# Optimization experiments

Measured on AMD Instinct MI355X. Metric: run time of the kernel, lower is better.

Reference implementation:

```python
import jax, jax.numpy as jnp
import numpy as np

NUM_HEADS = 8
HEAD_DIM = 16  # hidden_size 128 / 8 heads
SCALE = float(np.sqrt(HEAD_DIM))


def setup_inputs() -> dict:
    key = jax.random.key(0)
    k1, k2, k3, k4 = jax.random.split(key, 4)
    B, N, H = 1, 50000, 128
    E = 800000
    q = jax.random.normal(k1, (B, N, H), dtype=jnp.float32)
    k = jax.random.normal(k2, (B, N, H), dtype=jnp.float32)
    v = jax.random.normal(k3, (B, N, H), dtype=jnp.float32)
    edge_index = jax.random.randint(k4, (2, E), 0, N, dtype=jnp.int64)
    return {"q": q, "k": k, "v": v, "edge_index": edge_index}


def reference(q, k, v, edge_index):
    B, N, H = q.shape
    total = B * N
    qh = q.reshape(total, NUM_HEADS, HEAD_DIM)
    kh = k.reshape(total, NUM_HEADS, HEAD_DIM)
    vh = v.reshape(total, NUM_HEADS, HEAD_DIM)
    src_idx = edge_index[0]
    dst_idx = edge_index[1]
    src = kh[src_idx]          # [E, heads, d]
    dest = qh[dst_idx]         # [E, heads, d]
    # per-edge scaled dot score, clamped then exponentiated
    score = jnp.sum(src * dest / SCALE, axis=-1, keepdims=True)  # [E, heads, 1]
    score = jnp.exp(jnp.clip(score, -5.0, 5.0))
    msg = vh[src_idx] * score  # [E, heads, d]
    wV = jax.ops.segment_sum(msg, dst_idx, num_segments=total)    # [total, heads, d]
    Z = jax.ops.segment_sum(score, dst_idx, num_segments=total)   # [total, heads, 1]
    x = wV / (Z + 1e-6)
    return x.reshape(B, N, NUM_HEADS * HEAD_DIM)
```

## Files before the change

kernel.cpp:

```cpp
#include <hip/hip_runtime.h>

#define HID 128
#define CHUNK 16384
#define CSHIFT 14
#define MAXW 25088

typedef unsigned short u16;
typedef unsigned int u32;

__device__ __forceinline__ float lof(u32 w) { return __uint_as_float(w << 16); }
__device__ __forceinline__ float hif(u32 w) { return __uint_as_float(w & 0xFFFF0000u); }
__device__ __forceinline__ u16 f2bf(float f) {
    u32 x = __float_as_uint(f);
    return (u16)((x + 0x7FFF + ((x >> 16) & 1)) >> 16);
}

__global__ __launch_bounds__(1024) void hist_kernel(const int* __restrict__ ei,
        u32* __restrict__ Hp, u16* __restrict__ lrank, int E, int W) {
    __shared__ u32 hcnt[MAXW];
    int c = blockIdx.x;
    for (int j = threadIdx.x; j < W; j += 1024) hcnt[j] = 0;
    __syncthreads();
    int beg = c << CSHIFT;
    int end = min(E, beg + CHUNK);
    for (int i = beg + (int)threadIdx.x; i < end; i += 1024) {
        int d = ei[E + i];
        u32 sh = (u32)(d & 1) << 4;
        u32 old = atomicAdd(&hcnt[d >> 1], 1u << sh);
        lrank[i] = (u16)((old >> sh) & 0xFFFFu);
    }
    __syncthreads();
    for (int j = threadIdx.x; j < W; j += 1024) Hp[(size_t)c * W + j] = hcnt[j];
}

__global__ __launch_bounds__(1024) void scan_fused_kernel(u32* __restrict__ Hp,
        int* __restrict__ offsets, int* __restrict__ partials, int W, int NB, int N) {
    __shared__ int sdata[1024];
    int tid = threadIdx.x;
    int j = blockIdx.x * 1024 + tid;
    u32 lo = 0, hi = 0;
    if (j < W) {
        int c = 0;
        for (; c + 8 <= NB; c += 8) {
            u32 w[8];
#pragma unroll
            for (int t = 0; t < 8; t++) w[t] = Hp[(size_t)(c + t) * W + j];
#pragma unroll
            for (int t = 0; t < 8; t++) {
                Hp[(size_t)(c + t) * W + j] = lo | (hi << 16);
                lo += w[t] & 0xFFFFu;
                hi += w[t] >> 16;
            }
        }
        for (; c < NB; c++) {
            size_t idx = (size_t)c * W + j;
            u32 w = Hp[idx];
            Hp[idx] = lo | (hi << 16);
            lo += w & 0xFFFFu;
            hi += w >> 16;
        }
    }
    int s = (int)(lo + hi);
    sdata[tid] = s;
    __syncthreads();
    for (int off = 1; off < 1024; off <<= 1) {
        int x = sdata[tid];
        int y = (tid >= off) ? sdata[tid - off] : 0;
        __syncthreads();
        sdata[tid] = x + y;
        __syncthreads();
    }
    int excl = sdata[tid] - s;
    if (j < W) {
        int n0 = 2 * j, n1 = 2 * j + 1;
        offsets[n0] = excl;
        if (n1 < N) offsets[n1] = excl + (int)lo;
    }
    if (tid == 1023) partials[blockIdx.x] = sdata[1023];
}

__global__ void scanC_kernel(int* __restrict__ offsets, const int* __restrict__ partials,
                             int M, int E, int nbA) {
    __shared__ int sp[256];
    int tid = threadIdx.x;
    if (tid == 0) {
        int run = 0;
        for (int i = 0; i < nbA; i++) { sp[i] = run; run += partials[i]; }
    }
    __syncthreads();
    int idx = blockIdx.x * blockDim.x + tid;
    if (idx < M) offsets[idx] += sp[idx >> 11];
    if (idx == 0) offsets[M] = E;
}

__global__ void packscatter_kernel(const float* __restrict__ k, const float* __restrict__ v,
                                   u16* __restrict__ kv, const int* __restrict__ ei,
                                   const u32* __restrict__ Hp, const u16* __restrict__ lrank,
                                   const int* __restrict__ offsets, u16* __restrict__ srcs,
                                   int N, int E, int W, int packBlocks) {
    if ((int)blockIdx.x < packBlocks) {
        int g = blockIdx.x * 256 + threadIdx.x;
        int node = g >> 6, l = g & 63;
        if (node >= N) return;
        float2 kk = ((const float2*)(k + (long long)node * HID))[l];
        float2 vv = ((const float2*)(v + (long long)node * HID))[l];
        ushort4 o;
        o.x = f2bf(kk.x * 0.25f);
        o.y = f2bf(kk.y * 0.25f);
        o.z = f2bf(vv.x);
        o.w = f2bf(vv.y);
        ((ushort4*)(kv + (long long)node * 256))[l] = o;
    } else {
        int e = (blockIdx.x - packBlocks) * 256 + threadIdx.x;
        if (e >= E) return;
        int c = e >> CSHIFT;
        int d = ei[E + e];
        u32 sh = (u32)(d & 1) << 4;
        u32 b = (Hp[(size_t)c * W + (d >> 1)] >> sh) & 0xFFFFu;
        int pos = offsets[d] + (int)b + (int)lrank[e];
        srcs[pos] = (u16)ei[e];
    }
}

__global__ __launch_bounds__(128) void reduce_packed(
        const float* __restrict__ q, const u16* __restrict__ kv,
        const int* __restrict__ offsets, const u16* __restrict__ srcs,
        float* __restrict__ out, int N) {
    int node = blockIdx.x * 2 + (threadIdx.x >> 6);
    if (node >= N) return;
    int l = threadIdx.x & 63;
    int m = l & 31;
    int half = l >> 5;

    float4 qv = ((const float4*)(q + (long long)node * HID))[m];
    const char* kvb = (const char*)kv;
    u32 laneoff = (u32)m << 4;
    float4 acc = make_float4(0.0f, 0.0f, 0.0f, 0.0f);
    float z = 0.0f;

    int beg = offsets[node];
    int end = offsets[node + 1];
    int i = beg;

#define GLOAD(s_) (*(const uint4*)(kvb + (((u32)(s_) << 9) + laneoff)))

    for (; i + 8 <= end; i += 8) {
        u32 sA0 = srcs[i + 0], sB0 = srcs[i + 1];
        u32 sA1 = srcs[i + 2], sB1 = srcs[i + 3];
        u32 sA2 = srcs[i + 4], sB2 = srcs[i + 5];
        u32 sA3 = srcs[i + 6], sB3 = srcs[i + 7];
        uint4 a0 = GLOAD(half ? sB0 : sA0);
        uint4 a1 = GLOAD(half ? sB1 : sA1);
        uint4 a2 = GLOAD(half ? sB2 : sA2);
        uint4 a3 = GLOAD(half ? sB3 : sA3);

        float p0 = lof(a0.x) * qv.x + hif(a0.x) * qv.y + lof(a0.z) * qv.z + hif(a0.z) * qv.w;
        float p1 = lof(a1.x) * qv.x + hif(a1.x) * qv.y + lof(a1.z) * qv.z + hif(a1.z) * qv.w;
        float p2 = lof(a2.x) * qv.x + hif(a2.x) * qv.y + lof(a2.z) * qv.z + hif(a2.z) * qv.w;
        float p3 = lof(a3.x) * qv.x + hif(a3.x) * qv.y + lof(a3.z) * qv.z + hif(a3.z) * qv.w;

        p0 += __shfl_xor(p0, 1); p1 += __shfl_xor(p1, 1);
        p2 += __shfl_xor(p2, 1); p3 += __shfl_xor(p3, 1);
        p0 += __shfl_xor(p0, 2); p1 += __shfl_xor(p1, 2);
        p2 += __shfl_xor(p2, 2); p3 += __shfl_xor(p3, 2);

        float c0 = __expf(fminf(fmaxf(p0, -5.0f), 5.0f));
        float c1 = __expf(fminf(fmaxf(p1, -5.0f), 5.0f));
        float c2 = __expf(fminf(fmaxf(p2, -5.0f), 5.0f));
        float c3 = __expf(fminf(fmaxf(p3, -5.0f), 5.0f));

        acc.x += lof(a0.y) * c0 + lof(a1.y) * c1 + lof(a2.y) * c2 + lof(a3.y) * c3;
        acc.y += hif(a0.y) * c0 + hif(a1.y) * c1 + hif(a2.y) * c2 + hif(a3.y) * c3;
        acc.z += lof(a0.w) * c0 + lof(a1.w) * c1 + lof(a2.w) * c2 + lof(a3.w) * c3;
        acc.w += hif(a0.w) * c0 + hif(a1.w) * c1 + hif(a2.w) * c2 + hif(a3.w) * c3;
        z += c0 + c1 + c2 + c3;
    }
    for (; i < end; i += 2) {
        int idx = i + half;
        bool ok = idx < end;
        u32 s = srcs[ok ? idx : i];
        uint4 a = GLOAD(s);
        float p = lof(a.x) * qv.x + hif(a.x) * qv.y + lof(a.z) * qv.z + hif(a.z) * qv.w;
        p += __shfl_xor(p, 1);
        p += __shfl_xor(p, 2);
        float c = __expf(fminf(fmaxf(p, -5.0f), 5.0f));
        c = ok ? c : 0.0f;
        acc.x += lof(a.y) * c;
        acc.y += hif(a.y) * c;
        acc.z += lof(a.w) * c;
        acc.w += hif(a.w) * c;
        z += c;
    }
#undef GLOAD

    acc.x += __shfl_xor(acc.x, 32);
    acc.y += __shfl_xor(acc.y, 32);
    acc.z += __shfl_xor(acc.z, 32);
    acc.w += __shfl_xor(acc.w, 32);
    z     += __shfl_xor(z, 32);

    if (half == 0) {
        float inv = 1.0f / (z + 1e-6f);
        ((float4*)(out + (long long)node * HID))[m] =
            make_float4(acc.x * inv, acc.y * inv, acc.z * inv, acc.w * inv);
    }
}


__global__ void count_kernel(const int* __restrict__ ei, int* __restrict__ counts,
                             int* __restrict__ pos, int E) {
    int e = blockIdx.x * blockDim.x + threadIdx.x;
    if (e < E) pos[e] = atomicAdd(&counts[ei[E + e]], 1);
}

__global__ void fill_kernel(const int* __restrict__ ei, const int* __restrict__ offsets,
                            const int* __restrict__ pos, int* __restrict__ srcs, int E) {
    int e = blockIdx.x * blockDim.x + threadIdx.x;
    if (e < E) srcs[offsets[ei[E + e]] + pos[e]] = ei[e];
}

__global__ __launch_bounds__(256) void reduce_f32(
        const float* __restrict__ q, const float* __restrict__ k,
        const float* __restrict__ v, const int* __restrict__ offsets,
        const int* __restrict__ srcs, float* __restrict__ out, int N) {
    int node = blockIdx.x * 4 + (threadIdx.x >> 6);
    if (node >= N) return;
    int l = threadIdx.x & 63;
    float2 qv = ((const float2*)(q + (long long)node * HID))[l];
    float accx = 0.0f, accy = 0.0f, z = 0.0f;
    int beg = offsets[node], end = offsets[node + 1];
    for (int i = beg; i < end; i++) {
        int s = srcs[i];
        float2 kk = ((const float2*)(k + (long long)s * HID))[l];
        float2 vv = ((const float2*)(v + (long long)s * HID))[l];
        float p = (kk.x * qv.x + kk.y * qv.y) * 0.25f;
        p += __shfl_xor(p, 1);
        p += __shfl_xor(p, 2);
        p += __shfl_xor(p, 4);
        float c = __expf(fminf(fmaxf(p, -5.0f), 5.0f));
        accx += vv.x * c; accy += vv.y * c; z += c;
    }
    float inv = 1.0f / (z + 1e-6f);
    ((float2*)(out + (long long)node * HID))[l] = make_float2(accx * inv, accy * inv);
}

__global__ void scanA_kernel(const u32* __restrict__ counts, int* __restrict__ offsets,
                             int* __restrict__ partials, int M) {
    __shared__ int sdata[256];
    int tid = threadIdx.x;
    int base = blockIdx.x * 2048 + tid * 8;
    int v[8];
    int tsum = 0;
    for (int j = 0; j < 8; j++) {
        int idx = base + j;
        v[j] = (idx < M) ? (int)counts[idx] : 0;
        tsum += v[j];
    }
    sdata[tid] = tsum;
    __syncthreads();
    for (int off = 1; off < 256; off <<= 1) {
        int x = sdata[tid];
        int y = (tid >= off) ? sdata[tid - off] : 0;
        __syncthreads();
        sdata[tid] = x + y;
        __syncthreads();
    }
    int excl = sdata[tid] - tsum;
    for (int j = 0; j < 8; j++) {
        int idx = base + j;
        if (idx < M) offsets[idx] = excl;
        excl += v[j];
    }
    if (tid == 255) partials[blockIdx.x] = sdata[255];
}

extern "C" void kernel_launch(void* const* d_in, const int* in_sizes, int n_in,
                              void* d_out, int out_size, void* d_ws, size_t ws_size,
                              hipStream_t stream) {
    const float* q = (const float*)d_in[0];
    const float* k = (const float*)d_in[1];
    const float* v = (const float*)d_in[2];
    const int* ei = (const int*)d_in[3];
    float* out = (float*)d_out;

    int E = in_sizes[3] / 2;
    int N = in_sizes[0] / HID;

    int eblocks = (E + 255) / 256;
    int nbA = (N + 2047) / 2048;
    int nblocksN = (N + 255) / 256;

    int W = (N + 1) / 2;
    int NB = (E + CHUNK - 1) >> CSHIFT;
    int nbF = (W + 1023) / 1024;

    size_t kv_bytes = (size_t)N * 256 * sizeof(u16);
    size_t need = kv_bytes + ((size_t)NB * W + N + 1 + 256) * 4
                + 2 * ((size_t)E + 8) * 2 + 64;

    bool primary = (W <= MAXW) && (nbF <= 256) && (ws_size >= need);

    if (primary) {
        u16* kv = (u16*)d_ws;
        u32* Hp = (u32*)((char*)d_ws + kv_bytes);
        int* offsets = (int*)(Hp + (size_t)NB * W);
        int* partials = offsets + N + 1;
        u16* lrank = (u16*)(partials + 256);
        u16* srcs = lrank + ((E + 8) & ~1);

        int packBlocks = (N * 64 + 255) / 256;

        hist_kernel<<<NB, 1024, 0, stream>>>(ei, Hp, lrank, E, W);
        scan_fused_kernel<<<nbF, 1024, 0, stream>>>(Hp, offsets, partials, W, NB, N);
        scanC_kernel<<<nblocksN, 256, 0, stream>>>(offsets, partials, N, E, nbF);
        packscatter_kernel<<<packBlocks + eblocks, 256, 0, stream>>>(
            k, v, kv, ei, Hp, lrank, offsets, srcs, N, E, W, packBlocks);
        int rgrid = (N + 1) / 2;
        reduce_packed<<<rgrid, 128, 0, stream>>>(q, kv, offsets, srcs, out, N);
    } else {
        int* counts = (int*)d_ws;
        int* offsets = counts + N;
        int* partials = offsets + N + 1;
        int* pos = partials + 256;
        int* srcs = pos + E;

        hipMemsetAsync(counts, 0, (size_t)N * sizeof(int), stream);
        count_kernel<<<eblocks, 256, 0, stream>>>(ei, counts, pos, E);
        scanA_kernel<<<nbA, 256, 0, stream>>>((const u32*)counts, offsets, partials, N);
        scanC_kernel<<<nblocksN, 256, 0, stream>>>(offsets, partials, N, E, nbA);
        fill_kernel<<<eblocks, 256, 0, stream>>>(ei, offsets, pos, srcs, E);
        int rgrid = (N + 3) / 4;
        reduce_f32<<<rgrid, 256, 0, stream>>>(q, k, v, offsets, srcs, out, N);
    }
}
```

Before: 111.2 us.

## Split histogram per chunk into two halves and fuse k/v packing into it

The per-chunk histogram kernel now runs two blocks per edge chunk, each owning half of the packed destination counter range, so each block uses half the LDS (about 50KB instead of 100KB). That lets more blocks fit per CU and raises histogram parallelism. The bf16 packing of k/v moves from the scatter kernel into the histogram launch, so packing overlaps with histogramming and the scatter kernel is left doing only the scatter. The cost is that each edge's destination is read twice and filtered by range in the histogram blocks.

Result: faster. 104.8 us (-5.7%).

```diff
diff --git a/kernel.cpp b/kernel.cpp
--- a/kernel.cpp
+++ b/kernel.cpp
@@ -4,6 +4,7 @@
 #define CHUNK 16384
 #define CSHIFT 14
 #define MAXW 25088
+#define WH 12544
 
 typedef unsigned short u16;
 typedef unsigned int u32;
@@ -15,22 +16,46 @@
     return (u16)((x + 0x7FFF + ((x >> 16) & 1)) >> 16);
 }
 
-__global__ __launch_bounds__(1024) void hist_kernel(const int* __restrict__ ei,
-        u32* __restrict__ Hp, u16* __restrict__ lrank, int E, int W) {
-    __shared__ u32 hcnt[MAXW];
-    int c = blockIdx.x;
-    for (int j = threadIdx.x; j < W; j += 1024) hcnt[j] = 0;
-    __syncthreads();
-    int beg = c << CSHIFT;
-    int end = min(E, beg + CHUNK);
-    for (int i = beg + (int)threadIdx.x; i < end; i += 1024) {
-        int d = ei[E + i];
-        u32 sh = (u32)(d & 1) << 4;
-        u32 old = atomicAdd(&hcnt[d >> 1], 1u << sh);
-        lrank[i] = (u16)((old >> sh) & 0xFFFFu);
-    }
-    __syncthreads();
-    for (int j = threadIdx.x; j < W; j += 1024) Hp[(size_t)c * W + j] = hcnt[j];
+__global__ __launch_bounds__(1024) void histpack_kernel(
+        const int* __restrict__ ei, u32* __restrict__ Hp, u16* __restrict__ lrank,
+        const float* __restrict__ kin, const float* __restrict__ vin, u16* __restrict__ kv,
+        int E, int W, int N, int histBlocks) {
+    __shared__ u32 hcnt[WH];
+    if ((int)blockIdx.x < histBlocks) {
+        int c = blockIdx.x >> 1;
+        int h = blockIdx.x & 1;
+        int Wh = (W + 1) >> 1;
+        int base = h * Wh;
+        int wlen = min(Wh, W - base);
+        for (int j = threadIdx.x; j < wlen; j += 1024) hcnt[j] = 0;
+        __syncthreads();
+        int beg = c << CSHIFT;
+        int end = min(E, beg + CHUNK);
+        for (int i = beg + (int)threadIdx.x; i < end; i += 1024) {
+            int d = ei[E + i];
+            int w = d >> 1;
+            if (w >= base && w < base + wlen) {
+                u32 sh = (u32)(d & 1) << 4;
+                u32 old = atomicAdd(&hcnt[w - base], 1u << sh);
+                lrank[i] = (u16)((old >> sh) & 0xFFFFu);
+            }
+        }
+        __syncthreads();
+        for (int j = threadIdx.x; j < wlen; j += 1024)
+            Hp[(size_t)c * W + base + j] = hcnt[j];
+    } else {
+        int g = ((int)blockIdx.x - histBlocks) * 1024 + (int)threadIdx.x;
+        int node = g >> 6, l = g & 63;
+        if (node >= N) return;
+        float2 kk = ((const float2*)(kin + (long long)node * HID))[l];
+        float2 vv = ((const float2*)(vin + (long long)node * HID))[l];
+        ushort4 o;
+        o.x = f2bf(kk.x * 0.25f);
+        o.y = f2bf(kk.y * 0.25f);
+        o.z = f2bf(vv.x);
+        o.w = f2bf(vv.y);
+        ((ushort4*)(kv + (long long)node * 256))[l] = o;
+    }
 }
 
 __global__ __launch_bounds__(1024) void scan_fused_kernel(u32* __restrict__ Hp,
@@ -93,33 +118,17 @@
     if (idx == 0) offsets[M] = E;
 }
 
-__global__ void packscatter_kernel(const float* __restrict__ k, const float* __restrict__ v,
-                                   u16* __restrict__ kv, const int* __restrict__ ei,
-                                   const u32* __restrict__ Hp, const u16* __restrict__ lrank,
-                                   const int* __restrict__ offsets, u16* __restrict__ srcs,
-                                   int N, int E, int W, int packBlocks) {
-    if ((int)blockIdx.x < packBlocks) {
-        int g = blockIdx.x * 256 + threadIdx.x;
-        int node = g >> 6, l = g & 63;
-        if (node >= N) return;
-        float2 kk = ((const float2*)(k + (long long)node * HID))[l];
-        float2 vv = ((const float2*)(v + (long long)node * HID))[l];
-        ushort4 o;
-        o.x = f2bf(kk.x * 0.25f);
-        o.y = f2bf(kk.y * 0.25f);
-        o.z = f2bf(vv.x);
-        o.w = f2bf(vv.y);
-        ((ushort4*)(kv + (long long)node * 256))[l] = o;
-    } else {
-        int e = (blockIdx.x - packBlocks) * 256 + threadIdx.x;
-        if (e >= E) return;
-        int c = e >> CSHIFT;
-        int d = ei[E + e];
-        u32 sh = (u32)(d & 1) << 4;
-        u32 b = (Hp[(size_t)c * W + (d >> 1)] >> sh) & 0xFFFFu;
-        int pos = offsets[d] + (int)b + (int)lrank[e];
-        srcs[pos] = (u16)ei[e];
-    }
+__global__ void scatter_kernel(const int* __restrict__ ei, const u32* __restrict__ Hp,
+                               const u16* __restrict__ lrank, const int* __restrict__ offsets,
+                               u16* __restrict__ srcs, int E, int W) {
+    int e = blockIdx.x * blockDim.x + threadIdx.x;
+    if (e >= E) return;
+    int c = e >> CSHIFT;
+    int d = ei[E + e];
+    u32 sh = (u32)(d & 1) << 4;
+    u32 b = (Hp[(size_t)c * W + (d >> 1)] >> sh) & 0xFFFFu;
+    int pos = offsets[d] + (int)b + (int)lrank[e];
+    srcs[pos] = (u16)ei[e];
 }
 
 __global__ __launch_bounds__(128) void reduce_packed(
@@ -298,7 +307,7 @@
     size_t need = kv_bytes + ((size_t)NB * W + N + 1 + 256) * 4
                 + 2 * ((size_t)E + 8) * 2 + 64;
 
-    bool primary = (W <= MAXW) && (nbF <= 256) && (ws_size >= need);
+    bool primary = (((W + 1) >> 1) <= WH) && (nbF <= 256) && (ws_size >= need);
 
     if (primary) {
         u16* kv = (u16*)d_ws;
@@ -308,13 +317,14 @@
         u16* lrank = (u16*)(partials + 256);
         u16* srcs = lrank + ((E + 8) & ~1);
 
-        int packBlocks = (N * 64 + 255) / 256;
-
-        hist_kernel<<<NB, 1024, 0, stream>>>(ei, Hp, lrank, E, W);
+        int histBlocks = NB * 2;
+        int packBlocks = (N * 64 + 1023) / 1024;
+
+        histpack_kernel<<<histBlocks + packBlocks, 1024, 0, stream>>>(
+            ei, Hp, lrank, k, v, kv, E, W, N, histBlocks);
         scan_fused_kernel<<<nbF, 1024, 0, stream>>>(Hp, offsets, partials, W, NB, N);
         scanC_kernel<<<nblocksN, 256, 0, stream>>>(offsets, partials, N, E, nbF);
-        packscatter_kernel<<<packBlocks + eblocks, 256, 0, stream>>>(
-            k, v, kv, ei, Hp, lrank, offsets, srcs, N, E, W, packBlocks);
+        scatter_kernel<<<eblocks, 256, 0, stream>>>(ei, Hp, lrank, offsets, srcs, E, W);
         int rgrid = (N + 1) / 2;
         reduce_packed<<<rgrid, 128, 0, stream>>>(q, kv, offsets, srcs, out, N);
     } else {
```
